# Optimization experiments

Hardware: AMD Instinct MI355X
Metric: run time of the kernel (lower is better)

The kernel has to match this reference:

```python
import jax, jax.numpy as jnp
import numpy as np
import math

E = 2048         # n_embd
H = 16           # num query head pairs (num_heads)
HKV = 8          # num_kv_heads
NREP = H // HKV  # 2
HD = E // H // 2 # head_dim = 64
DEPTH = 12
LAMBDA_INIT = 0.8 - 0.6 * math.exp(-0.3 * DEPTH)
EPS = 1e-6


def setup_inputs() -> dict:
    key = jax.random.key(0)
    ks = jax.random.split(key, 10)
    s = lambda fan_in: 1.0 / np.sqrt(fan_in)
    return {
        "x": jax.random.normal(ks[0], (2, 2048, E), jnp.float32),
        "Wq": jax.random.normal(ks[1], (E, E), jnp.float32) * s(E),
        "Wk": jax.random.normal(ks[2], (E, E // NREP), jnp.float32) * s(E),
        "Wv": jax.random.normal(ks[3], (E, E // NREP), jnp.float32) * s(E),
        "Wo": jax.random.normal(ks[4], (E, E), jnp.float32) * s(E),
        "lam_q1": jax.random.normal(ks[5], (HD,), jnp.float32) * 0.1,
        "lam_k1": jax.random.normal(ks[6], (HD,), jnp.float32) * 0.1,
        "lam_q2": jax.random.normal(ks[7], (HD,), jnp.float32) * 0.1,
        "lam_k2": jax.random.normal(ks[8], (HD,), jnp.float32) * 0.1,
        "g": jnp.ones((2 * HD,), jnp.float32),  # RMSNorm weight
    }


def _rotary(x, cos, sin):
    # x: [B, T, nh, HD]; cos/sin: [T, HD//2]
    d = x.shape[-1] // 2
    x1, x2 = x[..., :d], x[..., d:]
    c = cos[None, :, None, :]
    si = sin[None, :, None, :]
    return jnp.concatenate([x1 * c + x2 * si, -x1 * si + x2 * c], axis=-1)


def reference(x, Wq, Wk, Wv, Wo, lam_q1, lam_k1, lam_q2, lam_k2, g):
    B, T, _ = x.shape
    q = (x @ Wq).reshape(B, T, 2 * H, HD)
    k = (x @ Wk).reshape(B, T, 2 * HKV, HD)
    v = (x @ Wv).reshape(B, T, HKV, 2 * HD)

    inv_freq = 1.0 / (10000.0 ** (jnp.arange(0, HD, 2, dtype=jnp.float32) / HD))
    freqs = jnp.arange(T, dtype=jnp.float32)[:, None] * inv_freq[None, :]
    cos, sin = jnp.cos(freqs), jnp.sin(freqs)
    q = _rotary(q, cos, sin)
    k = _rotary(k, cos, sin)

    q = jnp.transpose(q, (0, 2, 1, 3)) * (HD ** -0.5)   # [B, 2H, T, HD]
    k = jnp.repeat(jnp.transpose(k, (0, 2, 1, 3)), NREP, axis=1)  # [B, 2H, T, HD]
    v = jnp.repeat(jnp.transpose(v, (0, 2, 1, 3)), NREP, axis=1)  # [B, H, T, 2HD]

    scores = jnp.einsum('bhtd,bhsd->bhts', q, k)
    scores = jnp.nan_to_num(scores)
    mask = jnp.triu(jnp.full((T, T), -jnp.inf, scores.dtype), 1)
    scores = scores + mask
    p = jax.nn.softmax(scores.astype(jnp.float32), axis=-1).astype(scores.dtype)

    lam1 = jnp.exp(jnp.sum(lam_q1 * lam_k1))
    lam2 = jnp.exp(jnp.sum(lam_q2 * lam_k2))
    lam = lam1 - lam2 + LAMBDA_INIT

    p = p.reshape(B, H, 2, T, T)
    diff = p[:, :, 0] - lam * p[:, :, 1]               # [B, H, T, T]
    attn = jnp.einsum('bhts,bhsd->bhtd', diff, v)      # [B, H, T, 2HD]

    # RMSNorm over last dim (2*HD)
    attn = attn * jax.lax.rsqrt(jnp.mean(attn * attn, axis=-1, keepdims=True) + EPS) * g
    attn = attn * (1.0 - LAMBDA_INIT)
    attn = jnp.transpose(attn, (0, 2, 1, 3)).reshape(B, T, E)
    return attn @ Wo
```

## Files before the change

### kernel.cpp

```cpp
#include <hip/hip_runtime.h>

#define T_SEQ 2048

typedef __bf16 bf16x8 __attribute__((ext_vector_type(8)));
typedef float f32x4 __attribute__((ext_vector_type(4)));
typedef unsigned short u16;

__device__ __forceinline__ u16 f2b(float f) {
  unsigned u = __float_as_uint(f);
  unsigned r = 0x7fffu + ((u >> 16) & 1u);
  return (u16)((u + r) >> 16);
}
__device__ __forceinline__ float b2f(u16 v) {
  return __uint_as_float(((unsigned)v) << 16);
}
__device__ __forceinline__ f32x4 mfma16(bf16x8 a, bf16x8 b, f32x4 c) {
  return __builtin_amdgcn_mfma_f32_16x16x32_bf16(a, b, c, 0, 0, 0);
}
__device__ __forceinline__ unsigned pkhi(float lo, float hi) {
  return __builtin_amdgcn_perm(__float_as_uint(hi), __float_as_uint(lo), 0x07060302u);
}
__device__ __forceinline__ void glds16(const void* g, void* s) {
  __builtin_amdgcn_global_load_lds(
      (const __attribute__((address_space(1))) void*)(uintptr_t)g,
      (__attribute__((address_space(3))) void*)(unsigned)(uintptr_t)s, 16, 0, 0);
}

__global__ void lam_kernel(const float* __restrict__ q1, const float* __restrict__ k1,
                           const float* __restrict__ q2, const float* __restrict__ k2,
                           float* __restrict__ outp) {
  int l = threadIdx.x;
  float a = q1[l] * k1[l];
  float c = q2[l] * k2[l];
  #pragma unroll
  for (int off = 32; off > 0; off >>= 1) {
    a += __shfl_down(a, off);
    c += __shfl_down(c, off);
  }
  if (l == 0) outp[0] = expf(a) - expf(c) + 0.7836057665316244f;
}

__global__ __launch_bounds__(256) void convert_kernel(const float* __restrict__ in,
                                                      u16* __restrict__ outp, int n) {
  int i = (blockIdx.x * 256 + threadIdx.x) * 4;
  if (i >= n) return;
  float4 v = *(const float4*)(in + i);
  ushort4 pk;
  pk.x = f2b(v.x); pk.y = f2b(v.y); pk.z = f2b(v.z); pk.w = f2b(v.w);
  *(ushort4*)(outp + i) = pk;
}

__global__ __launch_bounds__(256) void transpose_kernel(const float* __restrict__ in,
                                                        u16* __restrict__ outp, int R, int C) {
  __shared__ float tile[32][33];
  int c0 = blockIdx.x * 32, r0 = blockIdx.y * 32;
  int tx = threadIdx.x & 31, ty = threadIdx.x >> 5;
  #pragma unroll
  for (int k2 = 0; k2 < 4; k2++)
    tile[ty * 4 + k2][tx] = in[(size_t)(r0 + ty * 4 + k2) * C + c0 + tx];
  __syncthreads();
  #pragma unroll
  for (int k2 = 0; k2 < 4; k2++)
    outp[(size_t)(c0 + ty * 4 + k2) * R + r0 + tx] = f2b(tile[tx][ty * 4 + k2]);
}

template <bool OUT_BF16>
__global__ __launch_bounds__(256) void gemm128_kernel(const u16* __restrict__ A,
                                                      const u16* __restrict__ BT,
                                                      void* __restrict__ C, int N, int K) {
  __shared__ alignas(16) u16 As[128 * 64];
  __shared__ alignas(16) u16 Bs[128 * 64];
  const int tid = threadIdx.x, w = tid >> 6, lane = tid & 63;
  const int l15 = lane & 15, quad = lane >> 4;
  const int m0 = blockIdx.y * 128, n0 = blockIdx.x * 128;
  const int wm = (w >> 1) * 64, wn = (w & 1) * 64;
  const int lr = lane >> 3, slot = lane & 7, csw = slot ^ lr;
  f32x4 acc[4][4];
  #pragma unroll
  for (int mt = 0; mt < 4; mt++)
    #pragma unroll
    for (int nt = 0; nt < 4; nt++) acc[mt][nt] = (f32x4){0.f, 0.f, 0.f, 0.f};
  const u16* Ag = A + (size_t)(m0 + w * 32 + lr) * K + csw * 8;
  const u16* Bg = BT + (size_t)(n0 + w * 32 + lr) * K + csw * 8;
  u16* Asd = As + (w * 32) * 64;
  u16* Bsd = Bs + (w * 32) * 64;
  for (int kt = 0; kt < K; kt += 64) {
    #pragma unroll
    for (int i = 0; i < 4; i++) {
      glds16(Ag + kt + (size_t)(i * 8) * K, Asd + i * 512);
      glds16(Bg + kt + (size_t)(i * 8) * K, Bsd + i * 512);
    }
    __syncthreads();
    #pragma unroll
    for (int kk = 0; kk < 2; kk++) {
      bf16x8 am[4], bn[4];
      #pragma unroll
      for (int t = 0; t < 4; t++) {
        const int ra = wm + t * 16 + l15;
        am[t] = *(const bf16x8*)&As[ra * 64 + (((kk * 4 + quad) ^ (ra & 7)) << 3)];
        const int rb = wn + t * 16 + l15;
        bn[t] = *(const bf16x8*)&Bs[rb * 64 + (((kk * 4 + quad) ^ (rb & 7)) << 3)];
      }
      #pragma unroll
      for (int mt = 0; mt < 4; mt++)
        #pragma unroll
        for (int nt = 0; nt < 4; nt++) acc[mt][nt] = mfma16(am[mt], bn[nt], acc[mt][nt]);
    }
    __syncthreads();
  }
  const int row = m0 + wm + quad * 4;
  #pragma unroll
  for (int mt = 0; mt < 4; mt++) {
    #pragma unroll
    for (int nt = 0; nt < 4; nt++) {
      const int col = n0 + wn + nt * 16 + l15;
      #pragma unroll
      for (int rr = 0; rr < 4; rr++) {
        if (OUT_BF16)
          ((u16*)C)[(size_t)(row + mt * 16 + rr) * N + col] = f2b(acc[mt][nt][rr]);
        else
          ((float*)C)[(size_t)(row + mt * 16 + rr) * N + col] = acc[mt][nt][rr];
      }
    }
  }
}

__global__ __launch_bounds__(256) void rotary_kernel(const u16* __restrict__ qkv,
                                                     u16* __restrict__ outp, int lh,
                                                     int colbase, float scale) {
  int idx = blockIdx.x * 256 + threadIdx.x;
  int i = idx & 31;
  int h = (idx >> 5) & ((1 << lh) - 1);
  int bt = idx >> (5 + lh);
  int t = bt & (T_SEQ - 1);
  size_t inb = (size_t)bt * 4096 + colbase + h * 64 + i;
  float x1 = b2f(qkv[inb]);
  float x2 = b2f(qkv[inb + 32]);
  float invf = exp2f(-(float)i * 0.4152410118609203f);
  float ang = (float)t * invf;
  float c = cosf(ang), s = sinf(ang);
  float o1 = (x1 * c + x2 * s) * scale;
  float o2 = (x2 * c - x1 * s) * scale;
  size_t ob = ((size_t)((bt >> 11) * (1 << lh) + h) * T_SEQ + t) * 64 + i;
  outp[ob] = f2b(o1);
  outp[ob + 32] = f2b(o2);
}

__global__ __launch_bounds__(256) void vtrans_kernel(const u16* __restrict__ qkv,
                                                     u16* __restrict__ outp) {
  __shared__ unsigned tile[32][33];
  int bh = blockIdx.z;
  int t0 = blockIdx.x * 32, dv0 = blockIdx.y * 32;
  int tx = threadIdx.x & 31, ty = threadIdx.x >> 5;
  int bt_base = (bh >> 3) * T_SEQ;
  int col = 3072 + (bh & 7) * 128 + dv0 + tx;
  #pragma unroll
  for (int k2 = 0; k2 < 4; k2++)
    tile[ty * 4 + k2][tx] = qkv[(size_t)(bt_base + t0 + ty * 4 + k2) * 4096 + col];
  __syncthreads();
  #pragma unroll
  for (int k2 = 0; k2 < 4; k2++)
    outp[((size_t)bh * 128 + dv0 + ty * 4 + k2) * T_SEQ + t0 + tx] = (u16)tile[tx][ty * 4 + k2];
}

__global__ __launch_bounds__(256) void attn_kernel(const u16* __restrict__ Qb,
                                                   const u16* __restrict__ Kb,
                                                   const u16* __restrict__ Vt,
                                                   const float* __restrict__ lamp,
                                                   const float* __restrict__ g,
                                                   u16* __restrict__ attn_out) {
  __shared__ alignas(16) u16 Ks[64 * 64];
  __shared__ alignas(16) u16 Vs[128 * 64];
  __shared__ alignas(16) u16 Ps[4][16][136];
  const int pr = blockIdx.x;
  const int bh = blockIdx.y;
  const int b = bh >> 4, h = bh & 15;
  const int tid = threadIdx.x, w = tid >> 6, lane = tid & 63;
  const int l15 = lane & 15, quad = lane >> 4;
  const int lr = lane >> 3, slot = lane & 7, csw = slot ^ lr;
  const float lam = lamp[0];

  const u16* Kbase = Kb + (size_t)(b * 16 + h) * T_SEQ * 64;
  const u16* Vbase = Vt + (size_t)(b * 8 + (h >> 1)) * 128 * T_SEQ;
  const u16* Kg = Kbase + (size_t)(w * 16 + lr) * 64 + csw * 8;
  const u16* Vg = Vbase + (size_t)(w * 32 + lr) * T_SEQ + csw * 8;

  #pragma unroll 1
  for (int half = 0; half < 2; half++) {
    const int tt = half ? 31 - pr : pr;
    const int qb = tt * 64 + w * 16;
    const int qglob = qb + l15;

    bf16x8 qf[2][2];
    #pragma unroll
    for (int e = 0; e < 2; e++)
      #pragma unroll
      for (int kk = 0; kk < 2; kk++)
        qf[e][kk] = *(const bf16x8*)&Qb[((size_t)(b * 32 + 2 * h + e) * T_SEQ + qb + l15) * 64 +
                                        kk * 32 + quad * 8];

    f32x4 o[2][8];
    float lsum[2] = {0.f, 0.f};
    #pragma unroll
    for (int e = 0; e < 2; e++)
      #pragma unroll
      for (int nt = 0; nt < 8; nt++) o[e][nt] = (f32x4){0.f, 0.f, 0.f, 0.f};

    for (int st = 0; st <= tt; st++) {
      const int s0 = st * 64;
      glds16(Kg + (size_t)s0 * 64, &Ks[(w * 16) * 64]);
      glds16(Kg + (size_t)(s0 + 8) * 64, &Ks[(w * 16 + 8) * 64]);
      #pragma unroll
      for (int i = 0; i < 4; i++)
        glds16(Vg + s0 + (size_t)(i * 8) * T_SEQ, &Vs[(w * 32 + i * 8) * 64]);
      __syncthreads();

      bf16x8 kf[4][2];
      #pragma unroll
      for (int j = 0; j < 4; j++) {
        const int rk = j * 16 + l15;
        #pragma unroll
        for (int kk = 0; kk < 2; kk++)
          kf[j][kk] = *(const bf16x8*)&Ks[rk * 64 + (((kk * 4 + quad) ^ (rk & 7)) << 3)];
      }

      #pragma unroll
      for (int e = 0; e < 2; e++) {
        f32x4 sc[4];
        #pragma unroll
        for (int j = 0; j < 4; j++) {
          f32x4 z = {0.f, 0.f, 0.f, 0.f};
          z = mfma16(kf[j][0], qf[e][0], z);
          sc[j] = mfma16(kf[j][1], qf[e][1], z);
        }
        if (st == tt) {
          #pragma unroll
          for (int j = 0; j < 4; j++) {
            int srow = s0 + j * 16 + quad * 4;
            #pragma unroll
            for (int rr = 0; rr < 4; rr++)
              if (srow + rr > qglob) sc[j][rr] = -1e30f;
          }
        }
        float ls = 0.f;
        #pragma unroll
        for (int j = 0; j < 4; j++) {
          #pragma unroll
          for (int rr = 0; rr < 4; rr++) {
            float p = exp2f(sc[j][rr]);
            sc[j][rr] = p;
            ls += p;
          }
          uint2 pk;
          pk.x = pkhi(sc[j][0], sc[j][1]);
          pk.y = pkhi(sc[j][2], sc[j][3]);
          *(uint2*)&Ps[w][l15][e * 64 + j * 16 + quad * 4] = pk;
        }
        lsum[e] += ls;
      }
      asm volatile("s_waitcnt lgkmcnt(0)" ::: "memory");
      bf16x8 pa[2][2];
      #pragma unroll
      for (int e = 0; e < 2; e++)
        #pragma unroll
        for (int kk = 0; kk < 2; kk++)
          pa[e][kk] = *(const bf16x8*)&Ps[w][l15][e * 64 + kk * 32 + quad * 8];
      asm volatile("" ::: "memory");
      #pragma unroll
      for (int nt = 0; nt < 8; nt++) {
        const int rv = nt * 16 + l15;
        bf16x8 vf0 = *(const bf16x8*)&Vs[rv * 64 + ((quad ^ (rv & 7)) << 3)];
        bf16x8 vf1 = *(const bf16x8*)&Vs[rv * 64 + (((4 + quad) ^ (rv & 7)) << 3)];
        o[0][nt] = mfma16(vf0, pa[0][0], o[0][nt]);
        o[0][nt] = mfma16(vf1, pa[0][1], o[0][nt]);
        o[1][nt] = mfma16(vf0, pa[1][0], o[1][nt]);
        o[1][nt] = mfma16(vf1, pa[1][1], o[1][nt]);
      }
      __syncthreads();
    }

    float l0 = lsum[0], l1 = lsum[1];
    l0 += __shfl_xor(l0, 16); l0 += __shfl_xor(l0, 32);
    l1 += __shfl_xor(l1, 16); l1 += __shfl_xor(l1, 32);
    const float il0 = 1.f / l0, il1 = lam / l1;
    float ssq = 0.f;
    #pragma unroll
    for (int nt = 0; nt < 8; nt++)
      #pragma unroll
      for (int rr = 0; rr < 4; rr++) {
        float v = o[0][nt][rr] * il0 - o[1][nt][rr] * il1;
        o[0][nt][rr] = v;
        ssq += v * v;
      }
    ssq += __shfl_xor(ssq, 16);
    ssq += __shfl_xor(ssq, 32);
    const float rsc = rsqrtf(ssq * (1.f / 128.f) + 1e-6f) * 0.2163942334683756f;
    #pragma unroll
    for (int nt = 0; nt < 8; nt++) {
      float4 gv = *(const float4*)&g[nt * 16 + quad * 4];
      uint2 pk;
      pk.x = (unsigned)f2b(o[0][nt][0] * rsc * gv.x) |
             ((unsigned)f2b(o[0][nt][1] * rsc * gv.y) << 16);
      pk.y = (unsigned)f2b(o[0][nt][2] * rsc * gv.z) |
             ((unsigned)f2b(o[0][nt][3] * rsc * gv.w) << 16);
      *(uint2*)&Ps[w][l15][nt * 16 + quad * 4] = pk;
    }
    asm volatile("s_waitcnt lgkmcnt(0)" ::: "memory");
    #pragma unroll
    for (int i = 0; i < 4; i++) {
      const int r = (lane >> 4) + i * 4, c = (lane & 15) * 8;
      bf16x8 ov = *(const bf16x8*)&Ps[w][r][c];
      *(bf16x8*)&attn_out[(size_t)(b * T_SEQ + qb + r) * 2048 + h * 128 + c] = ov;
    }
    __syncthreads();
  }
}

extern "C" void kernel_launch(void* const* d_in, const int* in_sizes, int n_in, void* d_out,
                              int out_size, void* d_ws, size_t ws_size, hipStream_t stream) {
  const float* x = (const float*)d_in[0];
  const float* Wq = (const float*)d_in[1];
  const float* Wk = (const float*)d_in[2];
  const float* Wv = (const float*)d_in[3];
  const float* Wo = (const float*)d_in[4];
  const float* lq1 = (const float*)d_in[5];
  const float* lk1 = (const float*)d_in[6];
  const float* lq2 = (const float*)d_in[7];
  const float* lk2 = (const float*)d_in[8];
  const float* g = (const float*)d_in[9];

  char* ws = (char*)d_ws;
  u16* WT = (u16*)(ws);
  u16* WoT = (u16*)(ws + 16777216);
  u16* xbf = (u16*)(ws + 25165824);
  u16* QKV = (u16*)(ws + 41943040);
  u16* Qb = (u16*)(ws + 75497472);
  u16* Kb = (u16*)(ws + 92274688);
  u16* Vt = (u16*)(ws + 100663296);
  u16* Attn = (u16*)(ws + 109051904);
  float* lam = (float*)(ws + 125829120);

  lam_kernel<<<1, 64, 0, stream>>>(lq1, lk1, lq2, lk2, lam);
  convert_kernel<<<8192, 256, 0, stream>>>(x, xbf, 8388608);
  transpose_kernel<<<dim3(64, 64), 256, 0, stream>>>(Wq, WT, 2048, 2048);
  transpose_kernel<<<dim3(32, 64), 256, 0, stream>>>(Wk, WT + (size_t)2048 * 2048, 2048, 1024);
  transpose_kernel<<<dim3(32, 64), 256, 0, stream>>>(Wv, WT + (size_t)3072 * 2048, 2048, 1024);
  transpose_kernel<<<dim3(64, 64), 256, 0, stream>>>(Wo, WoT, 2048, 2048);
  gemm128_kernel<true><<<dim3(32, 32), 256, 0, stream>>>(xbf, WT, QKV, 4096, 2048);
  rotary_kernel<<<16384, 256, 0, stream>>>(QKV, Qb, 5, 0, 0.18033688011112042f);
  rotary_kernel<<<8192, 256, 0, stream>>>(QKV, Kb, 4, 2048, 1.0f);
  vtrans_kernel<<<dim3(64, 4, 16), 256, 0, stream>>>(QKV, Vt);
  attn_kernel<<<dim3(16, 32), 256, 0, stream>>>(Qb, Kb, Vt, lam, g, Attn);
  gemm128_kernel<false><<<dim3(16, 32), 256, 0, stream>>>(Attn, WoT, d_out, 2048, 2048);
}
```

Before: 386.0 us.

## Double-buffer K/V tiles in attention and retile V transpose for contiguous loads

The attention inner loop now ping-pongs between two LDS buffers for K and V, so the next tile is issued with global_load_lds while the current one is being computed. This replaces the load-then-sync pattern, which left global latency exposed. The V-transpose kernel writes V in per-64-token tiles so each tile's loads are contiguous, and exp2f is swapped for the raw hardware v_exp_f32. The cost is doubled K/V LDS use, which may lower occupancy, plus hand-managed waitcnt/barrier sequencing that could race if it is wrong.

```diff
diff --git a/kernel.cpp b/kernel.cpp
--- a/kernel.cpp
+++ b/kernel.cpp
@@ -19,6 +19,20 @@
 }
 __device__ __forceinline__ unsigned pkhi(float lo, float hi) {
   return __builtin_amdgcn_perm(__float_as_uint(hi), __float_as_uint(lo), 0x07060302u);
+}
+#if defined(__has_builtin)
+#if __has_builtin(__builtin_amdgcn_exp2f)
+#define HAVE_RAW_EXP2 1
+#endif
+#endif
+__device__ __forceinline__ float exp2r(float x) {
+#ifdef HAVE_RAW_EXP2
+  return __builtin_amdgcn_exp2f(x);
+#else
+  float r;
+  asm("v_exp_f32 %0, %1" : "=v"(r) : "v"(x));
+  return r;
+#endif
 }
 __device__ __forceinline__ void glds16(const void* g, void* s) {
   __builtin_amdgcn_global_load_lds(
@@ -158,9 +172,12 @@
   for (int k2 = 0; k2 < 4; k2++)
     tile[ty * 4 + k2][tx] = qkv[(size_t)(bt_base + t0 + ty * 4 + k2) * 4096 + col];
   __syncthreads();
-  #pragma unroll
-  for (int k2 = 0; k2 < 4; k2++)
-    outp[((size_t)bh * 128 + dv0 + ty * 4 + k2) * T_SEQ + t0 + tx] = (u16)tile[tx][ty * 4 + k2];
+  const int stile = t0 >> 6, sin = (t0 & 63) + tx;
+  #pragma unroll
+  for (int k2 = 0; k2 < 4; k2++) {
+    int dv = dv0 + ty * 4 + k2;
+    outp[(((size_t)bh * 32 + stile) * 128 + dv) * 64 + sin] = (u16)tile[tx][ty * 4 + k2];
+  }
 }
 
 __global__ __launch_bounds__(256) void attn_kernel(const u16* __restrict__ Qb,
@@ -169,8 +186,8 @@
                                                    const float* __restrict__ lamp,
                                                    const float* __restrict__ g,
                                                    u16* __restrict__ attn_out) {
-  __shared__ alignas(16) u16 Ks[64 * 64];
-  __shared__ alignas(16) u16 Vs[128 * 64];
+  __shared__ alignas(16) u16 Ks[2][64 * 64];
+  __shared__ alignas(16) u16 Vs[2][128 * 64];
   __shared__ alignas(16) u16 Ps[4][16][136];
   const int pr = blockIdx.x;
   const int bh = blockIdx.y;
@@ -180,10 +197,12 @@
   const int lr = lane >> 3, slot = lane & 7, csw = slot ^ lr;
   const float lam = lamp[0];
 
-  const u16* Kbase = Kb + (size_t)(b * 16 + h) * T_SEQ * 64;
-  const u16* Vbase = Vt + (size_t)(b * 8 + (h >> 1)) * 128 * T_SEQ;
-  const u16* Kg = Kbase + (size_t)(w * 16 + lr) * 64 + csw * 8;
-  const u16* Vg = Vbase + (size_t)(w * 32 + lr) * T_SEQ + csw * 8;
+  u16* kd[2] = {&Ks[0][w * 1024], &Ks[1][w * 1024]};
+  u16* vd[2] = {&Vs[0][w * 2048], &Vs[1][w * 2048]};
+  const u16* KgBase =
+      Kb + (size_t)(b * 16 + h) * (T_SEQ * 64) + (w * 16 + lr) * 64 + csw * 8;
+  const u16* VgBase =
+      Vt + (size_t)(b * 8 + (h >> 1)) * (T_SEQ * 128) + w * 2048 + lr * 64 + csw * 8;
 
   #pragma unroll 1
   for (int half = 0; half < 2; half++) {
@@ -199,6 +218,13 @@
         qf[e][kk] = *(const bf16x8*)&Qb[((size_t)(b * 32 + 2 * h + e) * T_SEQ + qb + l15) * 64 +
                                         kk * 32 + quad * 8];
 
+    const u16* Kp = KgBase;
+    const u16* Vp = VgBase;
+    glds16(Kp, kd[0]); glds16(Kp + 512, kd[0] + 512);
+    glds16(Vp, vd[0]); glds16(Vp + 512, vd[0] + 512);
+    glds16(Vp + 1024, vd[0] + 1024); glds16(Vp + 1536, vd[0] + 1536);
+    Kp += 4096; Vp += 8192;
+
     f32x4 o[2][8];
     float lsum[2] = {0.f, 0.f};
     #pragma unroll
@@ -206,24 +232,25 @@
       #pragma unroll
       for (int nt = 0; nt < 8; nt++) o[e][nt] = (f32x4){0.f, 0.f, 0.f, 0.f};
 
-    for (int st = 0; st <= tt; st++) {
+    int st = 0;
+    auto step = [&](const u16* KC, const u16* VC, u16* KDN, u16* VDN) {
+      asm volatile("s_waitcnt vmcnt(0)" ::: "memory");
+      asm volatile("s_barrier" ::: "memory");
+      if (st < tt) {
+        glds16(Kp, KDN); glds16(Kp + 512, KDN + 512);
+        glds16(Vp, VDN); glds16(Vp + 512, VDN + 512);
+        glds16(Vp + 1024, VDN + 1024); glds16(Vp + 1536, VDN + 1536);
+        Kp += 4096; Vp += 8192;
+      }
       const int s0 = st * 64;
-      glds16(Kg + (size_t)s0 * 64, &Ks[(w * 16) * 64]);
-      glds16(Kg + (size_t)(s0 + 8) * 64, &Ks[(w * 16 + 8) * 64]);
-      #pragma unroll
-      for (int i = 0; i < 4; i++)
-        glds16(Vg + s0 + (size_t)(i * 8) * T_SEQ, &Vs[(w * 32 + i * 8) * 64]);
-      __syncthreads();
-
       bf16x8 kf[4][2];
       #pragma unroll
       for (int j = 0; j < 4; j++) {
         const int rk = j * 16 + l15;
         #pragma unroll
         for (int kk = 0; kk < 2; kk++)
-          kf[j][kk] = *(const bf16x8*)&Ks[rk * 64 + (((kk * 4 + quad) ^ (rk & 7)) << 3)];
-      }
-
+          kf[j][kk] = *(const bf16x8*)&KC[rk * 64 + (((kk * 4 + quad) ^ (rk & 7)) << 3)];
+      }
       #pragma unroll
       for (int e = 0; e < 2; e++) {
         f32x4 sc[4];
@@ -247,7 +274,7 @@
         for (int j = 0; j < 4; j++) {
           #pragma unroll
           for (int rr = 0; rr < 4; rr++) {
-            float p = exp2f(sc[j][rr]);
+            float p = exp2r(sc[j][rr]);
             sc[j][rr] = p;
             ls += p;
           }
@@ -269,15 +296,21 @@
       #pragma unroll
       for (int nt = 0; nt < 8; nt++) {
         const int rv = nt * 16 + l15;
-        bf16x8 vf0 = *(const bf16x8*)&Vs[rv * 64 + ((quad ^ (rv & 7)) << 3)];
-        bf16x8 vf1 = *(const bf16x8*)&Vs[rv * 64 + (((4 + quad) ^ (rv & 7)) << 3)];
+        bf16x8 vf0 = *(const bf16x8*)&VC[rv * 64 + ((quad ^ (rv & 7)) << 3)];
+        bf16x8 vf1 = *(const bf16x8*)&VC[rv * 64 + (((4 + quad) ^ (rv & 7)) << 3)];
         o[0][nt] = mfma16(vf0, pa[0][0], o[0][nt]);
         o[0][nt] = mfma16(vf1, pa[0][1], o[0][nt]);
         o[1][nt] = mfma16(vf0, pa[1][0], o[1][nt]);
         o[1][nt] = mfma16(vf1, pa[1][1], o[1][nt]);
       }
-      __syncthreads();
-    }
+    };
+    while (true) {
+      step(Ks[0], Vs[0], kd[1], vd[1]);
+      if (++st > tt) break;
+      step(Ks[1], Vs[1], kd[0], vd[0]);
+      if (++st > tt) break;
+    }
+    asm volatile("s_barrier" ::: "memory");
 
     float l0 = lsum[0], l1 = lsum[1];
     l0 += __shfl_xor(l0, 16); l0 += __shfl_xor(l0, 32);
@@ -312,7 +345,6 @@
       bf16x8 ov = *(const bf16x8*)&Ps[w][r][c];
       *(bf16x8*)&attn_out[(size_t)(b * T_SEQ + qb + r) * 2048 + h * 128 + c] = ov;
     }
-    __syncthreads();
   }
 }
 
```

Measured after the change: 396.4 us. 2.7% more time.
